# Kernel tuning notes

Hardware: AMD Instinct MI355X
Metric: run time of the kernel (lower is better)

## Reference

```python
import jax, jax.numpy as jnp
import numpy as np

KSIZE = 21


def extract_patches(x, k):
    """[b,c,h,w] -> [b,c,k*k,oh,ow], valid-mode ksize x ksize patches.

    Equivalent to torch x.unfold(2,k,1).unfold(3,k,1).reshape(b,c,oh,ow,k*k)
    (kernel offsets flattened row-major), with offset axis placed at dim 2.
    """
    b, c, h, w = x.shape
    p = jax.lax.conv_general_dilated_patches(x, (k, k), (1, 1), 'VALID')
    # output feature dim is ordered (c, kh, kw) -> reshape splits it cleanly
    return p.reshape(b, c, k * k, h - k + 1, w - k + 1)


def setup_inputs() -> dict:
    key = jax.random.key(0)
    k1, k2, k3 = jax.random.split(key, 3)
    b, c, h, w = 4, 3, 192, 192
    kernel_raw = jax.random.normal(k1, (b, KSIZE * KSIZE, h, w), jnp.float32)
    radiance = jax.random.uniform(k2, (b, c, h, w), dtype=jnp.float32)
    # sampling mask is binary {0,1} in the original
    mask = (jax.random.uniform(k3, (b, 1, h, w)) > 0.5).astype(jnp.float32)
    return {"kernel_raw": kernel_raw, "radiance": radiance, "mask": mask}


def reference(kernel_raw, radiance, mask):
    k = KSIZE
    b, c, h, w = radiance.shape
    kernel = jax.nn.softplus(kernel_raw)              # [b, k*k, h, w]
    # needed = h + k - 1 > h  ->  crop kernel by (k-1)//2 per side
    crop = (k - 1) // 2
    kernel = kernel[:, :, crop:h - crop, crop:w - crop]  # [b, k*k, kh, kw]
    tiles = extract_patches(radiance, k)               # [b, c, k*k, kh, kw]
    mtiles = extract_patches(mask, k)                  # [b, 1, k*k, kh, kw]
    kmask = kernel[:, None] * mtiles                   # masked per-pixel kernel
    weighted_sum = jnp.sum(kmask * tiles, axis=2)      # [b, c, kh, kw]
    kernel_sum = jnp.sum(kmask, axis=2)                # [b, 1, kh, kw]
    return weighted_sum, kernel_sum
```

## Files before the change

### kernel.cpp

```cpp
#include <hip/hip_runtime.h>
#include <hip/hip_bf16.h>

#define KS    21
#define H     192
#define W     192
#define OH    172
#define OW    172
#define CROP  10
#define PLANE (H*W)

#define NCHUNK 7
#define CROWS  3

#define TXD   16
#define TYD   8
#define TILE_W 32
#define TILE_H 8
#define SROWS (TILE_H + CROWS - 1)
#define SCOLS (TILE_W + KS - 1)
#define SCH   (SCOLS / 2)

#define CS    (OH * OW)
#define OUTN  (4 * 4 * OH * OW)

__device__ __forceinline__ float softplusf_(float x) {
    float e = __expf(-fabsf(x));
    return fmaxf(x, 0.0f) + __logf(1.0f + e);
}

#define LOADROW(buf, irow) do {                                              \
    const float* kp_ = kb + (size_t)(i0 + (irow)) * KS * PLANE;              \
    _Pragma("unroll")                                                        \
    for (int j = 0; j < KS; ++j)                                             \
        (buf)[j] = *reinterpret_cast<const float2*>(kp_ + (size_t)j * PLANE);\
} while (0)

#define COMPROW(buf, irow) do {                                              \
    const int rr_ = ty + (irow);                                             \
    float4 cur_ = s4[0][rr_][tx];                                            \
    _Pragma("unroll")                                                        \
    for (int j = 0; j < KS; ++j) {                                           \
        float4 nxt_ = s4[(j + 1) & 1][rr_][tx + ((j + 1) >> 1)];             \
        float s0_ = softplusf_((buf)[j].x);                                  \
        float s1_ = softplusf_((buf)[j].y);                                  \
        float km0_ = s0_ * cur_.x;                                           \
        float km1_ = s1_ * nxt_.x;                                           \
        ks0 += km0_;                                                         \
        ks1 += km1_;                                                         \
        a00 = fmaf(km0_, cur_.y, a00);  a01 = fmaf(km1_, nxt_.y, a01);       \
        a10 = fmaf(km0_, cur_.z, a10);  a11 = fmaf(km1_, nxt_.z, a11);       \
        a20 = fmaf(km0_, cur_.w, a20);  a21 = fmaf(km1_, nxt_.w, a21);       \
        cur_ = nxt_;                                                         \
    }                                                                        \
} while (0)

__global__ __launch_bounds__(TXD * TYD, 4)
void ar_partial_kernel(const float* __restrict__ kraw,
                       const float* __restrict__ rad,
                       const float* __restrict__ mask,
                       float* __restrict__ part)
{
    __shared__ float4 s4[2][SROWS][SCH];

    const int zz    = blockIdx.z;
    const int b     = zz & 3;
    const int chunk = zz >> 2;
    const int i0    = chunk * CROWS;

    const int x0t = blockIdx.x * TILE_W - CROP;
    const int y0t = blockIdx.y * TILE_H;
    const int tx  = threadIdx.x, ty = threadIdx.y;
    const int tid = ty * TXD + tx;

    const float* mbase = mask + (size_t)b * PLANE;
    const float* rbase = rad  + (size_t)b * 3 * PLANE;
    for (int t = tid; t < SROWS * SCOLS; t += TXD * TYD) {
        int rr = t / SCOLS, cc = t - rr * SCOLS;
        int gr = min(y0t + i0 + rr, H - 1);
        int gc = min(max(x0t + cc, 0), W - 1);
        int off = gr * W + gc;
        float4 v;
        v.x = mbase[off];
        v.y = rbase[off];
        v.z = rbase[off + PLANE];
        v.w = rbase[off + 2 * PLANE];
        s4[cc & 1][rr][cc >> 1] = v;
    }
    __syncthreads();

    const int x0 = x0t + tx * 2;
    const int y  = y0t + ty;

    const float* kb = kraw + (size_t)b * KS * KS * PLANE
                           + (size_t)(y + CROP) * W + (x0 + CROP);

    float ks0 = 0.f, ks1 = 0.f;
    float a00 = 0.f, a01 = 0.f;
    float a10 = 0.f, a11 = 0.f;
    float a20 = 0.f, a21 = 0.f;

    float2 kva[KS], kvb[KS];
    LOADROW(kva, 0);
    LOADROW(kvb, 1);
    COMPROW(kva, 0);
    LOADROW(kva, 2);
    COMPROW(kvb, 1);
    COMPROW(kva, 2);

    if (y < OH && x0 >= 0 && x0 < OW) {
        float* pb = part + (size_t)chunk * OUTN;
        const size_t wbase = ((size_t)b * 3 * OH + y) * OW + x0;
        const size_t kbase = (size_t)12 * CS + ((size_t)b * OH + y) * OW + x0;
        *reinterpret_cast<float2*>(pb + wbase)          = make_float2(a00, a01);
        *reinterpret_cast<float2*>(pb + wbase + CS)     = make_float2(a10, a11);
        *reinterpret_cast<float2*>(pb + wbase + 2 * CS) = make_float2(a20, a21);
        *reinterpret_cast<float2*>(pb + kbase)          = make_float2(ks0, ks1);
    }
}

__global__ __launch_bounds__(256)
void ar_reduce_kernel(const float* __restrict__ part, float* __restrict__ out)
{
    int i = blockIdx.x * 256 + threadIdx.x;
    if (i < OUTN / 4) {
        const float4* p4 = reinterpret_cast<const float4*>(part);
        float4 r = p4[i];
        #pragma unroll
        for (int k = 1; k < NCHUNK; ++k) {
            float4 v = p4[i + (size_t)k * (OUTN / 4)];
            r.x += v.x; r.y += v.y; r.z += v.z; r.w += v.w;
        }
        reinterpret_cast<float4*>(out)[i] = r;
    }
}

extern "C" void kernel_launch(void* const* d_in, const int* in_sizes, int n_in,
                              void* d_out, int out_size, void* d_ws, size_t ws_size,
                              hipStream_t stream) {
    const float* kraw = (const float*)d_in[0];
    const float* rad  = (const float*)d_in[1];
    const float* mask = (const float*)d_in[2];
    float* out  = (float*)d_out;
    float* part = (float*)d_ws;

    dim3 block(TXD, TYD, 1);
    dim3 grid((OW + TILE_W - 1) / TILE_W, (OH + TILE_H - 1) / TILE_H, 4 * NCHUNK);
    hipLaunchKernelGGL(ar_partial_kernel, grid, block, 0, stream,
                       kraw, rad, mask, part);

    int n4 = OUTN / 4;
    hipLaunchKernelGGL(ar_reduce_kernel, dim3((n4 + 255) / 256), dim3(256), 0, stream,
                       part, out);
}
```

Before: 61.99 us.

## Fuse chunk reduction into partial kernel via last-block atomic counter

Removes the separate reduce kernel. Each tile's last-arriving chunk block, detected with a per-tile atomic counter after a threadfence, sums the NCHUNK partials and writes the output. The first two kernel-row loads are also hoisted above the shared-memory fill so they overlap it. The cost is a memset launch for the counters, extra register pressure from issuing loads earlier, and serialized tail reduction work in the last blocks.

```diff
diff --git a/kernel.cpp b/kernel.cpp
--- a/kernel.cpp
+++ b/kernel.cpp
@@ -19,6 +19,10 @@
 #define SROWS (TILE_H + CROWS - 1)
 #define SCOLS (TILE_W + KS - 1)
 #define SCH   (SCOLS / 2)
+
+#define GX    6
+#define GY    22
+#define NTILES (GX * GY * 4)
 
 #define CS    (OH * OW)
 #define OUTN  (4 * 4 * OH * OW)
@@ -55,22 +59,36 @@
 } while (0)
 
 __global__ __launch_bounds__(TXD * TYD, 4)
-void ar_partial_kernel(const float* __restrict__ kraw,
-                       const float* __restrict__ rad,
-                       const float* __restrict__ mask,
-                       float* __restrict__ part)
+void ar_fused_kernel(const float* __restrict__ kraw,
+                     const float* __restrict__ rad,
+                     const float* __restrict__ mask,
+                     float* __restrict__ part,
+                     int* __restrict__ cnt,
+                     float* __restrict__ out)
 {
     __shared__ float4 s4[2][SROWS][SCH];
+    __shared__ int s_last;
 
     const int zz    = blockIdx.z;
     const int b     = zz & 3;
     const int chunk = zz >> 2;
     const int i0    = chunk * CROWS;
+    const int tileid = (b * GY + blockIdx.y) * GX + blockIdx.x;
 
     const int x0t = blockIdx.x * TILE_W - CROP;
     const int y0t = blockIdx.y * TILE_H;
     const int tx  = threadIdx.x, ty = threadIdx.y;
     const int tid = ty * TXD + tx;
+
+    const int x0 = x0t + tx * 2;
+    const int y  = y0t + ty;
+
+    const float* kb = kraw + (size_t)b * KS * KS * PLANE
+                           + (size_t)(y + CROP) * W + (x0 + CROP);
+
+    float2 kva[KS], kvb[KS];
+    LOADROW(kva, 0);
+    LOADROW(kvb, 1);
 
     const float* mbase = mask + (size_t)b * PLANE;
     const float* rbase = rad  + (size_t)b * 3 * PLANE;
@@ -88,49 +106,56 @@
     }
     __syncthreads();
 
-    const int x0 = x0t + tx * 2;
-    const int y  = y0t + ty;
-
-    const float* kb = kraw + (size_t)b * KS * KS * PLANE
-                           + (size_t)(y + CROP) * W + (x0 + CROP);
-
     float ks0 = 0.f, ks1 = 0.f;
     float a00 = 0.f, a01 = 0.f;
     float a10 = 0.f, a11 = 0.f;
     float a20 = 0.f, a21 = 0.f;
 
-    float2 kva[KS], kvb[KS];
-    LOADROW(kva, 0);
-    LOADROW(kvb, 1);
     COMPROW(kva, 0);
     LOADROW(kva, 2);
     COMPROW(kvb, 1);
     COMPROW(kva, 2);
 
-    if (y < OH && x0 >= 0 && x0 < OW) {
+    const bool valid = (y < OH) & (x0 >= 0) & (x0 < OW);
+    const size_t wbase = ((size_t)b * 3 * OH + y) * OW + x0;
+    const size_t kbase = (size_t)12 * CS + ((size_t)b * OH + y) * OW + x0;
+    if (valid) {
         float* pb = part + (size_t)chunk * OUTN;
-        const size_t wbase = ((size_t)b * 3 * OH + y) * OW + x0;
-        const size_t kbase = (size_t)12 * CS + ((size_t)b * OH + y) * OW + x0;
         *reinterpret_cast<float2*>(pb + wbase)          = make_float2(a00, a01);
         *reinterpret_cast<float2*>(pb + wbase + CS)     = make_float2(a10, a11);
         *reinterpret_cast<float2*>(pb + wbase + 2 * CS) = make_float2(a20, a21);
         *reinterpret_cast<float2*>(pb + kbase)          = make_float2(ks0, ks1);
     }
-}
 
-__global__ __launch_bounds__(256)
-void ar_reduce_kernel(const float* __restrict__ part, float* __restrict__ out)
-{
-    int i = blockIdx.x * 256 + threadIdx.x;
-    if (i < OUTN / 4) {
-        const float4* p4 = reinterpret_cast<const float4*>(part);
-        float4 r = p4[i];
-        #pragma unroll
-        for (int k = 1; k < NCHUNK; ++k) {
-            float4 v = p4[i + (size_t)k * (OUTN / 4)];
-            r.x += v.x; r.y += v.y; r.z += v.z; r.w += v.w;
+    __syncthreads();
+    if (tid == 0) {
+        __threadfence();
+        int old = atomicAdd(&cnt[tileid], 1);
+        s_last = (old == NCHUNK - 1);
+    }
+    __syncthreads();
+    if (s_last) {
+        __threadfence();
+        if (valid) {
+            float2 r0 = make_float2(0.f, 0.f), r1 = r0, r2 = r0, rk = r0;
+            #pragma unroll
+            for (int k = 0; k < NCHUNK; ++k) {
+                const float* pk = part + (size_t)k * OUTN;
+                float2 v;
+                v = *reinterpret_cast<const float2*>(pk + wbase);
+                r0.x += v.x; r0.y += v.y;
+                v = *reinterpret_cast<const float2*>(pk + wbase + CS);
+                r1.x += v.x; r1.y += v.y;
+                v = *reinterpret_cast<const float2*>(pk + wbase + 2 * CS);
+                r2.x += v.x; r2.y += v.y;
+                v = *reinterpret_cast<const float2*>(pk + kbase);
+                rk.x += v.x; rk.y += v.y;
+            }
+            *reinterpret_cast<float2*>(out + wbase)          = r0;
+            *reinterpret_cast<float2*>(out + wbase + CS)     = r1;
+            *reinterpret_cast<float2*>(out + wbase + 2 * CS) = r2;
+            *reinterpret_cast<float2*>(out + kbase)          = rk;
         }
-        reinterpret_cast<float4*>(out)[i] = r;
     }
 }
 
@@ -142,13 +167,12 @@
     const float* mask = (const float*)d_in[2];
     float* out  = (float*)d_out;
     float* part = (float*)d_ws;
+    int*   cnt  = (int*)((char*)d_ws + (size_t)NCHUNK * OUTN * sizeof(float));
+
+    hipMemsetAsync(cnt, 0, NTILES * sizeof(int), stream);
 
     dim3 block(TXD, TYD, 1);
-    dim3 grid((OW + TILE_W - 1) / TILE_W, (OH + TILE_H - 1) / TILE_H, 4 * NCHUNK);
-    hipLaunchKernelGGL(ar_partial_kernel, grid, block, 0, stream,
-                       kraw, rad, mask, part);
-
-    int n4 = OUTN / 4;
-    hipLaunchKernelGGL(ar_reduce_kernel, dim3((n4 + 255) / 256), dim3(256), 0, stream,
-                       part, out);
+    dim3 grid(GX, GY, 4 * NCHUNK);
+    hipLaunchKernelGGL(ar_fused_kernel, grid, block, 0, stream,
+                       kraw, rad, mask, part, cnt, out);
 }
```

After: 245.9 us. 297% more time.
